# Kernel optimization log

Measured on AMD Instinct MI355X. Metric: run time of the kernel, lower is better.

Reference implementation:

```python
import jax, jax.numpy as jnp
import numpy as np

L, B, C = 512, 64, 512  # seq_len, batch, tags_size


def setup_inputs() -> dict:
    key = jax.random.key(0)
    k1, k2, k3, k4, k5, k6 = jax.random.split(key, 6)
    std = (1.0 / C) ** 0.5
    emit = jax.random.normal(k1, (L, B, C), dtype=jnp.float32)
    trans = jax.random.normal(k2, (C, C), dtype=jnp.float32) * std
    trans_from_start = jax.random.normal(k3, (C,), dtype=jnp.float32) * std
    trans_to_end = jax.random.normal(k4, (C,), dtype=jnp.float32) * std
    target = jax.random.randint(k5, (L, B), 0, C)
    # left-aligned length mask so mask.sum(0)-1 indexes the last valid step
    lens = jax.random.randint(k6, (B,), L // 2, L + 1)
    mask = jnp.arange(L)[:, None] < lens[None, :]
    return {"emit": emit, "target": target, "mask": mask, "trans": trans,
            "trans_from_start": trans_from_start, "trans_to_end": trans_to_end}


def _log_z(emit, mask, trans, trans_from_start, trans_to_end):
    log_alpha0 = emit[0] + trans_from_start  # (B, C)

    def step(log_alpha, xs):
        e_i, m_i = xs  # (B, C), (B,)
        # scores[b, j] = logsumexp_i( log_alpha[b, i] + trans[i, j] + e_i[b, j] )
        s = jax.nn.logsumexp(log_alpha[:, :, None] + trans[None, :, :] + e_i[:, None, :], axis=1)
        log_alpha = jnp.where(m_i[:, None], s, log_alpha)
        return log_alpha, None

    log_alpha, _ = jax.lax.scan(step, log_alpha0, (emit[1:], mask[1:]))
    return jax.nn.logsumexp(log_alpha + trans_to_end, axis=1).sum()


def _score(emit, target, mask, trans, trans_from_start, trans_to_end):
    l, b, c = emit.shape
    tr = trans[target[:-1], target[1:]]  # (L-1, B)
    scores = jnp.concatenate([jnp.zeros((1, b), emit.dtype), tr], axis=0)
    scores = scores + jnp.take_along_axis(emit, target[:, :, None], axis=2)[..., 0]
    score = jnp.where(mask, scores, jnp.zeros((), emit.dtype)).sum()
    ends = mask.sum(axis=0) - 1  # (B,) index of last valid step
    last_tags = target[ends, jnp.arange(b)]
    score = score + trans_from_start[target[0]].sum() + trans_to_end[last_tags].sum()
    return score


def reference(emit, target, mask, trans, trans_from_start, trans_to_end):
    b = emit.shape[1]
    log_z = _log_z(emit, mask, trans, trans_from_start, trans_to_end)
    score = _score(emit, target, mask, trans, trans_from_start, trans_to_end)
    return (log_z - score) / b
```

## Files before the change

### kernel.cpp

```cpp
#include <hip/hip_runtime.h>
#include <hip/hip_bf16.h>
#include <stdint.h>

#define LL 512
#define BB 64
#define CC 512
#define TM 255

typedef float float4v __attribute__((ext_vector_type(4)));
typedef int   int4v   __attribute__((ext_vector_type(4)));
typedef unsigned int uint4v __attribute__((ext_vector_type(4)));
typedef int   int8v  __attribute__((ext_vector_type(8)));

#define WS_ET     262144
#define WS_SCORE  524288
#define WS_SVA    524292
#define WS_SVB    524548
#define WS_CTR    524804
#define WS_ALPHA  528384
#define WS_BETA   659456


__device__ __forceinline__ bool mask_at(const void* maskp, bool is_byte, int t, int b) {
    if (is_byte) return ((const unsigned char*)maskp)[t * BB + b] != 0;
    return ((const int*)maskp)[t * BB + b] != 0;
}

__device__ __forceinline__ float rowmax16_dpp(float x) {
    int t;
    t = __builtin_amdgcn_update_dpp(0, __float_as_int(x), 0x128, 0xF, 0xF, true);
    x = fmaxf(x, __int_as_float(t));
    t = __builtin_amdgcn_update_dpp(0, __float_as_int(x), 0x124, 0xF, 0xF, true);
    x = fmaxf(x, __int_as_float(t));
    t = __builtin_amdgcn_update_dpp(0, __float_as_int(x), 0x122, 0xF, 0xF, true);
    x = fmaxf(x, __int_as_float(t));
    t = __builtin_amdgcn_update_dpp(0, __float_as_int(x), 0x121, 0xF, 0xF, true);
    x = fmaxf(x, __int_as_float(t));
    return x;
}

__device__ __forceinline__ void step_barrier() {
    asm volatile("s_waitcnt lgkmcnt(0)" ::: "memory");
    __builtin_amdgcn_sched_barrier(0);
    __builtin_amdgcn_s_barrier();
    asm volatile("" ::: "memory");
}

__global__ void prep_kernel(const float* __restrict__ trans, unsigned char* __restrict__ ws) {
    int g = blockIdx.x * blockDim.x + threadIdx.x;
    if (g == 0) { *(float*)(ws + WS_SCORE) = 0.0f; *(int*)(ws + WS_CTR) = 0; }
    if (g >= 512 * 128) return;
    int n  = g & 511;
    int pd = g >> 9;
    int wv = pd >> 4, rw = pd & 15;
    float f[4], ft[4];
#pragma unroll
    for (int nt = 0; nt < 4; ++nt) {
        int k = 64 * wv + 16 * nt + rw;
        f[nt]  = __expf(trans[(size_t)k * CC + n]);
        ft[nt] = __expf(trans[(size_t)n * CC + k]);
    }
    int r = 0;
    r = __builtin_amdgcn_cvt_pk_fp8_f32(f[0], f[1], r, false);
    r = __builtin_amdgcn_cvt_pk_fp8_f32(f[2], f[3], r, true);
    ((int*)ws)[n * 128 + pd] = r;
    int r2 = 0;
    r2 = __builtin_amdgcn_cvt_pk_fp8_f32(ft[0], ft[1], r2, false);
    r2 = __builtin_amdgcn_cvt_pk_fp8_f32(ft[2], ft[3], r2, true);
    ((int*)(ws + WS_ET))[n * 128 + pd] = r2;
}

__launch_bounds__(512, 2)
__global__ void crf_scan_kernel(const float* __restrict__ emit,
                                const int* __restrict__ target,
                                const void* __restrict__ maskp,
                                const float* __restrict__ trans,
                                const float* __restrict__ tfs,
                                const float* __restrict__ t2e,
                                unsigned char* __restrict__ ws,
                                float* __restrict__ out) {
    const int tid = threadIdx.x;
    const bool is_byte = ((const unsigned char*)maskp)[1] != 0;

    if (blockIdx.x >= 8) {
        __shared__ float acc8[8];
        int sb = blockIdx.x - 8;
        float val = 0.0f;
        for (int e = sb * 512 + tid; e < LL * BB; e += 32 * 512) {
            int t = e >> 6, b = e & 63;
            if (mask_at(maskp, is_byte, t, b)) {
                int tg  = target[t * BB + b];
                float v = emit[(size_t)(t * BB + b) * CC + tg];
                if (t > 0) v += trans[(size_t)target[(t - 1) * BB + b] * CC + tg];
                val += v;
            }
        }
        if (sb == 0 && tid < BB) {
            int b = tid;
            val += tfs[target[b]];
            int lo = 0, hi = LL;
            while (lo < hi) {
                int mid = (lo + hi) >> 1;
                if (mask_at(maskp, is_byte, mid, b)) lo = mid + 1; else hi = mid;
            }
            val += t2e[target[(lo - 1) * BB + b]];
        }
        for (int off = 32; off > 0; off >>= 1) val += __shfl_down(val, off);
        if ((tid & 63) == 0) atomicAdd((float*)(ws + WS_SCORE), val);
        __syncthreads();
        if (tid == 0) { __threadfence(); atomicAdd((int*)(ws + WS_CTR), 1); }

        if (blockIdx.x == 39) {
            if (tid == 0) {
                while (atomicAdd((int*)(ws + WS_CTR), 0) < 40) __builtin_amdgcn_s_sleep(2);
                __threadfence();
            }
            __syncthreads();
            const int c  = tid >> 3;
            const int s8 = tid & 7;
            const float* A = (const float*)(ws + WS_ALPHA) + (size_t)c * CC;
            const float* B = (const float*)(ws + WS_BETA)  + (size_t)c * CC;
            float d = 0.0f;
            for (int i = s8; i < CC; i += 8) d += A[i] * B[i];
            d += __shfl_xor(d, 1);
            d += __shfl_xor(d, 2);
            d += __shfl_xor(d, 4);
            float v = 0.0f;
            if (s8 == 0)
                v = ((const float*)(ws + WS_SVA))[c] + ((const float*)(ws + WS_SVB))[c] + __logf(d);
            for (int off = 32; off > 0; off >>= 1) v += __shfl_down(v, off);
            if ((tid & 63) == 0) acc8[tid >> 6] = v;
            __syncthreads();
            if (tid == 0) {
                float s = 0.0f;
                for (int i = 0; i < 8; ++i) s += acc8[i];
                out[0] = (s - *(const float*)(ws + WS_SCORE)) * (1.0f / 64.0f);
            }
        }
        return;
    }

    const bool is_fwd = blockIdx.x < 4;
    const int B0 = (is_fwd ? blockIdx.x : blockIdx.x - 4) * 16;

    __shared__ __align__(16) unsigned char p8[2][16 * 528];
    __shared__ __align__(16) float mslotW[2][8][16];
    __shared__ float m0S[16];
    __shared__ float red[16][32];
    __shared__ int   lenS[16];
    __shared__ float mInitS;

    const int wv   = tid >> 6;
    const int lane = tid & 63;
    const int q    = lane >> 4;
    const int r15  = lane & 15;

    const unsigned char* ews = ws + (is_fwd ? 0 : WS_ET);
    int8v ef[4][4];
#pragma unroll
    for (int nt = 0; nt < 4; ++nt) {
        int n = (wv * 4 + nt) * 16 + r15;
#pragma unroll
        for (int kk4 = 0; kk4 < 4; ++kk4) {
            const unsigned char* src = ews + n * 512 + kk4 * 128 + q * 32;
            int4v lo = *(const int4v*)(src);
            int4v hi = *(const int4v*)(src + 16);
            ef[nt][kk4] = __builtin_shufflevector(lo, hi, 0, 1, 2, 3, 4, 5, 6, 7);
        }
    }

    const int c5 = tid >> 5;
    const int s5 = tid & 31;

    if (is_fwd) {
        {
            float lmax = -3.0e38f;
#pragma unroll
            for (int i = 0; i < 4; ++i) {
                int j4 = s5 + 32 * i;
                float4v em = *(const float4v*)(emit + (size_t)(B0 + c5) * CC + 4 * j4);
                float4v tf = *(const float4v*)(tfs + 4 * j4);
                float4v a = em + tf;
                lmax = fmaxf(lmax, fmaxf(fmaxf(a.x, a.y), fmaxf(a.z, a.w)));
            }
            red[c5][s5] = lmax;
        }
        __syncthreads();
        if (tid < 16) {
            float m0 = red[tid][0];
            for (int s = 1; s < 32; ++s) m0 = fmaxf(m0, red[tid][s]);
            m0S[tid] = m0;
        }
        if (tid < 128) ((float*)&mslotW[0][0][0])[tid] = 1.0f;
        __syncthreads();
        {
            float m0 = m0S[c5];
#pragma unroll
            for (int i = 0; i < 4; ++i) {
                int pd = s5 + 32 * i;
                int wvv = pd >> 4, rw = pd & 15;
                float f[4];
#pragma unroll
                for (int nt = 0; nt < 4; ++nt) {
                    int k = 64 * wvv + 16 * nt + rw;
                    f[nt] = __expf(emit[(size_t)(B0 + c5) * CC + k] + tfs[k] - m0);
                }
                int r = 0;
                r = __builtin_amdgcn_cvt_pk_fp8_f32(f[0], f[1], r, false);
                r = __builtin_amdgcn_cvt_pk_fp8_f32(f[2], f[3], r, true);
                *(int*)(&p8[0][0] + c5 * 528 + pd * 4) = r;
            }
        }
        __syncthreads();
    } else {
        {
            float m = t2e[tid];
            for (int off = 32; off > 0; off >>= 1) m = fmaxf(m, __shfl_xor(m, off));
            if (lane == 0) ((float*)red)[wv] = m;
        }
        __syncthreads();
        if (tid == 0) {
            float m = ((float*)red)[0];
            for (int i = 1; i < 8; ++i) m = fmaxf(m, ((float*)red)[i]);
            mInitS = __expf(m);
        }
        __syncthreads();
        {
#pragma unroll
            for (int i = 0; i < 4; ++i) {
                int pd = s5 + 32 * i;
                int wvv = pd >> 4, rw = pd & 15;
                float f[4];
#pragma unroll
                for (int nt = 0; nt < 4; ++nt)
                    f[nt] = __expf(t2e[64 * wvv + 16 * nt + rw]);
                int r = 0;
                r = __builtin_amdgcn_cvt_pk_fp8_f32(f[0], f[1], r, false);
                r = __builtin_amdgcn_cvt_pk_fp8_f32(f[2], f[3], r, true);
                *(int*)(&p8[0][0] + c5 * 528 + pd * 4) = r;
                *(int*)(&p8[1][0] + c5 * 528 + pd * 4) = r;
            }
            int part = 0;
            for (int k = 0; k < 16; ++k)
                part += mask_at(maskp, is_byte, s5 * 16 + k, B0 + c5) ? 1 : 0;
            red[c5][s5] = (float)part;
        }
        __syncthreads();
        if (tid < 16) {
            int s = 0;
            for (int i = 0; i < 32; ++i) s += (int)red[tid][i];
            lenS[tid] = s;
        }
        __syncthreads();
    }

    int4v gsum = {0, 0, 0, 0};
    const float4v z4 = {0.f, 0.f, 0.f, 0.f};

    if (is_fwd) {
        const float* eb0 = emit + (size_t)(BB + B0 + q * 4) * CC + (wv * 64 + r15);
        const float* eb1 = eb0 + 2 * CC;
        float4v ex4[4];
#pragma unroll
        for (int nt = 0; nt < 4; ++nt) {
            ex4[nt][0] = __expf(eb0[0 * CC + nt * 16]);
            ex4[nt][1] = __expf(eb0[1 * CC + nt * 16]);
            ex4[nt][2] = __expf(eb1[0 * CC + nt * 16]);
            ex4[nt][3] = __expf(eb1[1 * CC + nt * 16]);
        }

#pragma unroll 2
        for (int t = 1; t <= TM; ++t) {
            const int wp = t & 1;
            const int rp = wp ^ 1;
            eb0 += BB * CC;
            eb1 += BB * CC;

            const unsigned char* pr = &p8[rp][0] + r15 * 528 + q * 32;
            int8v af[4];
#pragma unroll
            for (int kk4 = 0; kk4 < 4; ++kk4) {
                int4v lo = *(const int4v*)(pr + kk4 * 128);
                int4v hi = *(const int4v*)(pr + kk4 * 128 + 16);
                af[kk4] = __builtin_shufflevector(lo, hi, 0, 1, 2, 3, 4, 5, 6, 7);
            }
            const char* mb = (const char*)&mslotW[(t - 1) & 1][0][q * 4];
            uint4v mm = *(const uint4v*)(mb);
#pragma unroll
            for (int i = 1; i < 8; ++i)
                mm = __builtin_elementwise_max(mm, *(const uint4v*)(mb + i * 64));

            float4v emn4[4];
#pragma unroll
            for (int nt = 0; nt < 4; ++nt) {
                emn4[nt][0] = eb0[0 * CC + nt * 16];
                emn4[nt][1] = eb0[1 * CC + nt * 16];
                emn4[nt][2] = eb1[0 * CC + nt * 16];
                emn4[nt][3] = eb1[1 * CC + nt * 16];
            }

            float4v acc0 = z4, acc1 = z4, acc2 = z4, acc3 = z4;
#pragma unroll
            for (int kk4 = 0; kk4 < 4; ++kk4) {
                acc0 = __builtin_amdgcn_mfma_scale_f32_16x16x128_f8f6f4(
                    af[kk4], ef[0][kk4], acc0, 0, 0, 0, 0x7F7F7F7F, 0, 0x7F7F7F7F);
                acc1 = __builtin_amdgcn_mfma_scale_f32_16x16x128_f8f6f4(
                    af[kk4], ef[1][kk4], acc1, 0, 0, 0, 0x7F7F7F7F, 0, 0x7F7F7F7F);
            }

            int4v e4 = {(int)(mm[0] >> 23), (int)(mm[1] >> 23), (int)(mm[2] >> 23), (int)(mm[3] >> 23)};
            int4v s2b = (248 - e4) << 23;
            float4v s24;
            s24[0] = __int_as_float(s2b[0]); s24[1] = __int_as_float(s2b[1]);
            s24[2] = __int_as_float(s2b[2]); s24[3] = __int_as_float(s2b[3]);

            float4v p0 = acc0 * (ex4[0] * s24);
            float4v p1 = acc1 * (ex4[1] * s24);
            float4v rmA = __builtin_elementwise_max(p0, p1);
            {
                unsigned char* wrow = &p8[wp][0] + (wv * 16 + r15) * 4;
#pragma unroll
                for (int rr = 0; rr < 4; ++rr) {
                    int r = __builtin_amdgcn_cvt_pk_fp8_f32(
                        fminf(p0[rr], 448.0f), fminf(p1[rr], 448.0f), 0, false);
                    *(short*)(wrow + (q * 4 + rr) * 528) = (short)r;
                }
            }
            ex4[0][0] = __expf(emn4[0][0]); ex4[0][1] = __expf(emn4[0][1]);
            ex4[0][2] = __expf(emn4[0][2]); ex4[0][3] = __expf(emn4[0][3]);
            ex4[1][0] = __expf(emn4[1][0]); ex4[1][1] = __expf(emn4[1][1]);
            ex4[1][2] = __expf(emn4[1][2]); ex4[1][3] = __expf(emn4[1][3]);

#pragma unroll
            for (int kk4 = 0; kk4 < 4; ++kk4) {
                acc2 = __builtin_amdgcn_mfma_scale_f32_16x16x128_f8f6f4(
                    af[kk4], ef[2][kk4], acc2, 0, 0, 0, 0x7F7F7F7F, 0, 0x7F7F7F7F);
                acc3 = __builtin_amdgcn_mfma_scale_f32_16x16x128_f8f6f4(
                    af[kk4], ef[3][kk4], acc3, 0, 0, 0, 0x7F7F7F7F, 0, 0x7F7F7F7F);
            }

            float4v p2 = acc2 * (ex4[2] * s24);
            float4v p3 = acc3 * (ex4[3] * s24);
            float4v rmB = __builtin_elementwise_max(p2, p3);
            {
                unsigned char* wrow = &p8[wp][0] + (wv * 16 + r15) * 4;
#pragma unroll
                for (int rr = 0; rr < 4; ++rr) {
                    int r = __builtin_amdgcn_cvt_pk_fp8_f32(
                        fminf(p2[rr], 448.0f), fminf(p3[rr], 448.0f), 0, false);
                    *(short*)(wrow + (q * 4 + rr) * 528 + 2) = (short)r;
                }
            }
            ex4[2][0] = __expf(emn4[2][0]); ex4[2][1] = __expf(emn4[2][1]);
            ex4[2][2] = __expf(emn4[2][2]); ex4[2][3] = __expf(emn4[2][3]);
            ex4[3][0] = __expf(emn4[3][0]); ex4[3][1] = __expf(emn4[3][1]);
            ex4[3][2] = __expf(emn4[3][2]); ex4[3][3] = __expf(emn4[3][3]);

            {
                float4v rm4 = __builtin_elementwise_max(rmA, rmB);
                float4v rw;
#pragma unroll
                for (int rr = 0; rr < 4; ++rr) rw[rr] = rowmax16_dpp(rm4[rr]);
                if (r15 == 0)
                    *(float4v*)&mslotW[t & 1][wv][q * 4] = rw;
            }

            gsum += (e4 - 121);

            if (t == TM) {
                float* wA = (float*)(ws + WS_ALPHA) + (size_t)(B0 + q * 4) * CC + (wv * 64 + r15);
#pragma unroll
                for (int rr = 0; rr < 4; ++rr) {
                    wA[(size_t)rr * CC +  0] = p0[rr];
                    wA[(size_t)rr * CC + 16] = p1[rr];
                    wA[(size_t)rr * CC + 32] = p2[rr];
                    wA[(size_t)rr * CC + 48] = p3[rr];
                }
            }
            step_barrier();
        }
        if (wv == 0 && r15 == 0) {
#pragma unroll
            for (int rr = 0; rr < 4; ++rr)
                ((float*)(ws + WS_SVA))[B0 + q * 4 + rr] =
                    m0S[q * 4 + rr] + 0.6931471805599453f * (float)gsum[rr];
        }
    } else {
        int lenR[4];
#pragma unroll
        for (int rr = 0; rr < 4; ++rr) lenR[rr] = lenS[q * 4 + rr];
        const int eInit = __float_as_int(mInitS) >> 23;

        int rInit = 0;
        rInit = __builtin_amdgcn_cvt_pk_fp8_f32(__expf(t2e[64 * wv + r15]),
                                                __expf(t2e[64 * wv + 16 + r15]), rInit, false);
        rInit = __builtin_amdgcn_cvt_pk_fp8_f32(__expf(t2e[64 * wv + 32 + r15]),
                                                __expf(t2e[64 * wv + 48 + r15]), rInit, true);
        const short rInitLo = (short)(rInit & 0xffff);
        const short rInitHi = (short)(((unsigned)rInit) >> 16);

        const float* eb0 = emit + ((size_t)(LL - 1) * BB + B0 + q * 4) * CC + (wv * 64 + r15);
        const float* eb1 = eb0 + 2 * CC;
        float4v ex4[4];
#pragma unroll
        for (int nt = 0; nt < 4; ++nt) {
            ex4[nt][0] = __expf(eb0[0 * CC + nt * 16]);
            ex4[nt][1] = __expf(eb0[1 * CC + nt * 16]);
            ex4[nt][2] = __expf(eb1[0 * CC + nt * 16]);
            ex4[nt][3] = __expf(eb1[1 * CC + nt * 16]);
        }

#pragma unroll 2
        for (int it = 0; it < 256; ++it) {
            const int t  = 510 - it;
            const int wp = it & 1;
            const int rp = wp ^ 1;
            eb0 -= BB * CC;
            eb1 -= BB * CC;

            const unsigned char* pr = &p8[rp][0] + r15 * 528 + q * 32;
            int8v af[4];
#pragma unroll
            for (int kk4 = 0; kk4 < 4; ++kk4) {
                int4v lo = *(const int4v*)(pr + kk4 * 128);
                int4v hi = *(const int4v*)(pr + kk4 * 128 + 16);
                af[kk4] = __builtin_shufflevector(lo, hi, 0, 1, 2, 3, 4, 5, 6, 7);
            }
            const char* mb = (const char*)&mslotW[(it - 1) & 1][0][q * 4];
            uint4v mm = *(const uint4v*)(mb);
#pragma unroll
            for (int i = 1; i < 8; ++i)
                mm = __builtin_elementwise_max(mm, *(const uint4v*)(mb + i * 64));

            float4v emn4[4];
#pragma unroll
            for (int nt = 0; nt < 4; ++nt) {
                emn4[nt][0] = eb0[0 * CC + nt * 16];
                emn4[nt][1] = eb0[1 * CC + nt * 16];
                emn4[nt][2] = eb1[0 * CC + nt * 16];
                emn4[nt][3] = eb1[1 * CC + nt * 16];
            }

            float4v acc0 = z4, acc1 = z4, acc2 = z4, acc3 = z4;
#pragma unroll
            for (int kk4 = 0; kk4 < 4; ++kk4) {
                acc0 = __builtin_amdgcn_mfma_scale_f32_16x16x128_f8f6f4(
                    af[kk4], ef[0][kk4], acc0, 0, 0, 0, 0x7F7F7F7F, 0, 0x7F7F7F7F);
                acc1 = __builtin_amdgcn_mfma_scale_f32_16x16x128_f8f6f4(
                    af[kk4], ef[1][kk4], acc1, 0, 0, 0, 0x7F7F7F7F, 0, 0x7F7F7F7F);
            }

            int4v e4 = {(int)(mm[0] >> 23), (int)(mm[1] >> 23), (int)(mm[2] >> 23), (int)(mm[3] >> 23)};
            int4v eU;
            float4v s2U;
            bool lv[4];
#pragma unroll
            for (int rr = 0; rr < 4; ++rr) {
                bool ui = (t >= lenR[rr] - 2);
                lv[rr] = (t <= lenR[rr] - 2);
                int e = ui ? eInit : e4[rr];
                eU[rr] = e;
                s2U[rr] = __int_as_float((248 - e) << 23);
            }

            float4v p0 = acc0 * (ex4[0] * s2U);
            float4v p1 = acc1 * (ex4[1] * s2U);
            float4v rmA = __builtin_elementwise_max(p0, p1);
            {
                unsigned char* wrow = &p8[wp][0] + (wv * 16 + r15) * 4;
#pragma unroll
                for (int rr = 0; rr < 4; ++rr) {
                    int r = __builtin_amdgcn_cvt_pk_fp8_f32(
                        fminf(p0[rr], 448.0f), fminf(p1[rr], 448.0f), 0, false);
                    *(short*)(wrow + (q * 4 + rr) * 528) = lv[rr] ? (short)r : rInitLo;
                }
            }
            ex4[0][0] = __expf(emn4[0][0]); ex4[0][1] = __expf(emn4[0][1]);
            ex4[0][2] = __expf(emn4[0][2]); ex4[0][3] = __expf(emn4[0][3]);
            ex4[1][0] = __expf(emn4[1][0]); ex4[1][1] = __expf(emn4[1][1]);
            ex4[1][2] = __expf(emn4[1][2]); ex4[1][3] = __expf(emn4[1][3]);

#pragma unroll
            for (int kk4 = 0; kk4 < 4; ++kk4) {
                acc2 = __builtin_amdgcn_mfma_scale_f32_16x16x128_f8f6f4(
                    af[kk4], ef[2][kk4], acc2, 0, 0, 0, 0x7F7F7F7F, 0, 0x7F7F7F7F);
                acc3 = __builtin_amdgcn_mfma_scale_f32_16x16x128_f8f6f4(
                    af[kk4], ef[3][kk4], acc3, 0, 0, 0, 0x7F7F7F7F, 0, 0x7F7F7F7F);
            }

            float4v p2 = acc2 * (ex4[2] * s2U);
            float4v p3 = acc3 * (ex4[3] * s2U);
            float4v rmB = __builtin_elementwise_max(p2, p3);
            {
                unsigned char* wrow = &p8[wp][0] + (wv * 16 + r15) * 4;
#pragma unroll
                for (int rr = 0; rr < 4; ++rr) {
                    int r = __builtin_amdgcn_cvt_pk_fp8_f32(
                        fminf(p2[rr], 448.0f), fminf(p3[rr], 448.0f), 0, false);
                    *(short*)(wrow + (q * 4 + rr) * 528 + 2) = lv[rr] ? (short)r : rInitHi;
                }
            }
            ex4[2][0] = __expf(emn4[2][0]); ex4[2][1] = __expf(emn4[2][1]);
            ex4[2][2] = __expf(emn4[2][2]); ex4[2][3] = __expf(emn4[2][3]);
            ex4[3][0] = __expf(emn4[3][0]); ex4[3][1] = __expf(emn4[3][1]);
            ex4[3][2] = __expf(emn4[3][2]); ex4[3][3] = __expf(emn4[3][3]);

            {
                float4v rm4 = __builtin_elementwise_max(rmA, rmB);
                float4v rw;
#pragma unroll
                for (int rr = 0; rr < 4; ++rr) rw[rr] = rowmax16_dpp(rm4[rr]);
                if (r15 == 0)
                    *(float4v*)&mslotW[it & 1][wv][q * 4] = rw;
            }

#pragma unroll
            for (int rr = 0; rr < 4; ++rr)
                gsum[rr] += lv[rr] ? (eU[rr] - 121) : 0;

            if (t == TM) {
                float* wB = (float*)(ws + WS_BETA) + (size_t)(B0 + q * 4) * CC + (wv * 64 + r15);
#pragma unroll
                for (int nt = 0; nt < 4; ++nt) {
                    float e2 = __expf(t2e[wv * 64 + nt * 16 + r15]);
                    const float4v& psel = (nt == 0) ? p0 : (nt == 1) ? p1 : (nt == 2) ? p2 : p3;
#pragma unroll
                    for (int rr = 0; rr < 4; ++rr)
                        wB[(size_t)rr * CC + nt * 16] = lv[rr] ? psel[rr] : e2;
                }
            }
            step_barrier();
        }
        if (wv == 0 && r15 == 0) {
#pragma unroll
            for (int rr = 0; rr < 4; ++rr)
                ((float*)(ws + WS_SVB))[B0 + q * 4 + rr] =
                    0.6931471805599453f * (float)gsum[rr];
        }
    }

    __syncthreads();
    if (tid == 0) { __threadfence(); atomicAdd((int*)(ws + WS_CTR), 1); }
}

extern "C" void kernel_launch(void* const* d_in, const int* in_sizes, int n_in,
                              void* d_out, int out_size, void* d_ws, size_t ws_size,
                              hipStream_t stream) {
    const float* emit   = (const float*)d_in[0];
    const int*   target = (const int*)d_in[1];
    const void*  maskp  = d_in[2];
    const float* trans  = (const float*)d_in[3];
    const float* tfs    = (const float*)d_in[4];
    const float* t2e    = (const float*)d_in[5];
    unsigned char* ws   = (unsigned char*)d_ws;
    float* out          = (float*)d_out;

    prep_kernel<<<256, 256, 0, stream>>>(trans, ws);
    crf_scan_kernel<<<40, 512, 0, stream>>>(emit, target, maskp, trans, tfs, t2e, ws, out);
}
```

Before: 567.3 us.

## Double scan block width to 16 waves, stream trans fragments from memory, split combine kernel

The forward/backward scan blocks go from 8 to 16 waves, so each wave handles 32 output tags (two MFMA tiles) instead of 64 per step. Transition fragments are no longer held in registers; they are reloaded each step from the workspace with software-prefetched double buffering. The final combine moves from a spin-waiting block into a separate small kernel, which removes the atomic counter. This aims to shorten the per-step critical path of the serial scan through more parallelism, at the cost of more global/L2 traffic per step and a wider cross-wave max reduction across 16 slots.

Result: slower. 2.062 ms (+263.4%).

```diff
diff --git a/kernel.cpp b/kernel.cpp
--- a/kernel.cpp
+++ b/kernel.cpp
@@ -14,9 +14,8 @@
 
 #define WS_ET     262144
 #define WS_SCORE  524288
-#define WS_SVA    524292
-#define WS_SVB    524548
-#define WS_CTR    524804
+#define WS_SVA    524352
+#define WS_SVB    524608
 #define WS_ALPHA  528384
 #define WS_BETA   659456
 
@@ -48,7 +47,7 @@
 
 __global__ void prep_kernel(const float* __restrict__ trans, unsigned char* __restrict__ ws) {
     int g = blockIdx.x * blockDim.x + threadIdx.x;
-    if (g == 0) { *(float*)(ws + WS_SCORE) = 0.0f; *(int*)(ws + WS_CTR) = 0; }
+    if (g == 0) *(float*)(ws + WS_SCORE) = 0.0f;
     if (g >= 512 * 128) return;
     int n  = g & 511;
     int pd = g >> 9;
@@ -70,23 +69,21 @@
     ((int*)(ws + WS_ET))[n * 128 + pd] = r2;
 }
 
-__launch_bounds__(512, 2)
+__launch_bounds__(1024, 4)
 __global__ void crf_scan_kernel(const float* __restrict__ emit,
                                 const int* __restrict__ target,
                                 const void* __restrict__ maskp,
                                 const float* __restrict__ trans,
                                 const float* __restrict__ tfs,
                                 const float* __restrict__ t2e,
-                                unsigned char* __restrict__ ws,
-                                float* __restrict__ out) {
+                                unsigned char* __restrict__ ws) {
     const int tid = threadIdx.x;
     const bool is_byte = ((const unsigned char*)maskp)[1] != 0;
 
     if (blockIdx.x >= 8) {
-        __shared__ float acc8[8];
         int sb = blockIdx.x - 8;
         float val = 0.0f;
-        for (int e = sb * 512 + tid; e < LL * BB; e += 32 * 512) {
+        for (int e = sb * 1024 + tid; e < LL * BB; e += 32 * 1024) {
             int t = e >> 6, b = e & 63;
             if (mask_at(maskp, is_byte, t, b)) {
                 int tg  = target[t * BB + b];
@@ -107,36 +104,6 @@
         }
         for (int off = 32; off > 0; off >>= 1) val += __shfl_down(val, off);
         if ((tid & 63) == 0) atomicAdd((float*)(ws + WS_SCORE), val);
-        __syncthreads();
-        if (tid == 0) { __threadfence(); atomicAdd((int*)(ws + WS_CTR), 1); }
-
-        if (blockIdx.x == 39) {
-            if (tid == 0) {
-                while (atomicAdd((int*)(ws + WS_CTR), 0) < 40) __builtin_amdgcn_s_sleep(2);
-                __threadfence();
-            }
-            __syncthreads();
-            const int c  = tid >> 3;
-            const int s8 = tid & 7;
-            const float* A = (const float*)(ws + WS_ALPHA) + (size_t)c * CC;
-            const float* B = (const float*)(ws + WS_BETA)  + (size_t)c * CC;
-            float d = 0.0f;
-            for (int i = s8; i < CC; i += 8) d += A[i] * B[i];
-            d += __shfl_xor(d, 1);
-            d += __shfl_xor(d, 2);
-            d += __shfl_xor(d, 4);
-            float v = 0.0f;
-            if (s8 == 0)
-                v = ((const float*)(ws + WS_SVA))[c] + ((const float*)(ws + WS_SVB))[c] + __logf(d);
-            for (int off = 32; off > 0; off >>= 1) v += __shfl_down(v, off);
-            if ((tid & 63) == 0) acc8[tid >> 6] = v;
-            __syncthreads();
-            if (tid == 0) {
-                float s = 0.0f;
-                for (int i = 0; i < 8; ++i) s += acc8[i];
-                out[0] = (s - *(const float*)(ws + WS_SCORE)) * (1.0f / 64.0f);
-            }
-        }
         return;
     }
 
@@ -144,7 +111,7 @@
     const int B0 = (is_fwd ? blockIdx.x : blockIdx.x - 4) * 16;
 
     __shared__ __align__(16) unsigned char p8[2][16 * 528];
-    __shared__ __align__(16) float mslotW[2][8][16];
+    __shared__ __align__(16) float mslotW[2][16][16];
     __shared__ float m0S[16];
     __shared__ float red[16][32];
     __shared__ int   lenS[16];
@@ -154,26 +121,11 @@
     const int lane = tid & 63;
     const int q    = lane >> 4;
     const int r15  = lane & 15;
-
-    const unsigned char* ews = ws + (is_fwd ? 0 : WS_ET);
-    int8v ef[4][4];
-#pragma unroll
-    for (int nt = 0; nt < 4; ++nt) {
-        int n = (wv * 4 + nt) * 16 + r15;
-#pragma unroll
-        for (int kk4 = 0; kk4 < 4; ++kk4) {
-            const unsigned char* src = ews + n * 512 + kk4 * 128 + q * 32;
-            int4v lo = *(const int4v*)(src);
-            int4v hi = *(const int4v*)(src + 16);
-            ef[nt][kk4] = __builtin_shufflevector(lo, hi, 0, 1, 2, 3, 4, 5, 6, 7);
-        }
-    }
-
-    const int c5 = tid >> 5;
-    const int s5 = tid & 31;
+    const int c5   = tid >> 5;
+    const int s5   = tid & 31;
 
     if (is_fwd) {
-        {
+        if (tid < 512) {
             float lmax = -3.0e38f;
 #pragma unroll
             for (int i = 0; i < 4; ++i) {
@@ -191,9 +143,9 @@
             for (int s = 1; s < 32; ++s) m0 = fmaxf(m0, red[tid][s]);
             m0S[tid] = m0;
         }
-        if (tid < 128) ((float*)&mslotW[0][0][0])[tid] = 1.0f;
-        __syncthreads();
-        {
+        if (tid < 256) ((float*)&mslotW[0][0][0])[tid] = 1.0f;
+        __syncthreads();
+        if (tid < 512) {
             float m0 = m0S[c5];
 #pragma unroll
             for (int i = 0; i < 4; ++i) {
@@ -213,7 +165,7 @@
         }
         __syncthreads();
     } else {
-        {
+        if (tid < 512) {
             float m = t2e[tid];
             for (int off = 32; off > 0; off >>= 1) m = fmaxf(m, __shfl_xor(m, off));
             if (lane == 0) ((float*)red)[wv] = m;
@@ -225,7 +177,7 @@
             mInitS = __expf(m);
         }
         __syncthreads();
-        {
+        if (tid < 512) {
 #pragma unroll
             for (int i = 0; i < 4; ++i) {
                 int pd = s5 + 32 * i;
@@ -254,59 +206,42 @@
         __syncthreads();
     }
 
+    const unsigned char* ews = ws + (is_fwd ? 0 : WS_ET);
+    const unsigned char* pA = ews + (size_t)(wv * 32 + r15) * 512 + q * 32;
+    const unsigned char* pB = pA + 16 * 512;
+    const int wcol = (wv >> 1) * 64 + r15 * 4 + (wv & 1) * 2;
+
     int4v gsum = {0, 0, 0, 0};
     const float4v z4 = {0.f, 0.f, 0.f, 0.f};
 
     if (is_fwd) {
-        const float* eb0 = emit + (size_t)(BB + B0 + q * 4) * CC + (wv * 64 + r15);
+        const float* eb0 = emit + (size_t)(BB + B0 + q * 4) * CC + (wv * 32 + r15);
         const float* eb1 = eb0 + 2 * CC;
-        float4v ex4[4];
-#pragma unroll
-        for (int nt = 0; nt < 4; ++nt) {
-            ex4[nt][0] = __expf(eb0[0 * CC + nt * 16]);
-            ex4[nt][1] = __expf(eb0[1 * CC + nt * 16]);
-            ex4[nt][2] = __expf(eb1[0 * CC + nt * 16]);
-            ex4[nt][3] = __expf(eb1[1 * CC + nt * 16]);
-        }
-
-#pragma unroll 2
+        float exv[8];
+        exv[0] = __expf(eb0[0]);  exv[1] = __expf(eb0[CC]);
+        exv[2] = __expf(eb1[0]);  exv[3] = __expf(eb1[CC]);
+        exv[4] = __expf(eb0[16]); exv[5] = __expf(eb0[CC + 16]);
+        exv[6] = __expf(eb1[16]); exv[7] = __expf(eb1[CC + 16]);
+
+#pragma unroll 1
         for (int t = 1; t <= TM; ++t) {
-            const int wp = t & 1;
-            const int rp = wp ^ 1;
+            const int wp = t & 1, rp = wp ^ 1;
             eb0 += BB * CC;
             eb1 += BB * CC;
 
             const unsigned char* pr = &p8[rp][0] + r15 * 528 + q * 32;
-            int8v af[4];
-#pragma unroll
-            for (int kk4 = 0; kk4 < 4; ++kk4) {
-                int4v lo = *(const int4v*)(pr + kk4 * 128);
-                int4v hi = *(const int4v*)(pr + kk4 * 128 + 16);
-                af[kk4] = __builtin_shufflevector(lo, hi, 0, 1, 2, 3, 4, 5, 6, 7);
-            }
+
             const char* mb = (const char*)&mslotW[(t - 1) & 1][0][q * 4];
             uint4v mm = *(const uint4v*)(mb);
 #pragma unroll
-            for (int i = 1; i < 8; ++i)
+            for (int i = 1; i < 16; ++i)
                 mm = __builtin_elementwise_max(mm, *(const uint4v*)(mb + i * 64));
 
-            float4v emn4[4];
-#pragma unroll
-            for (int nt = 0; nt < 4; ++nt) {
-                emn4[nt][0] = eb0[0 * CC + nt * 16];
-                emn4[nt][1] = eb0[1 * CC + nt * 16];
-                emn4[nt][2] = eb1[0 * CC + nt * 16];
-                emn4[nt][3] = eb1[1 * CC + nt * 16];
-            }
-
-            float4v acc0 = z4, acc1 = z4, acc2 = z4, acc3 = z4;
-#pragma unroll
-            for (int kk4 = 0; kk4 < 4; ++kk4) {
-                acc0 = __builtin_amdgcn_mfma_scale_f32_16x16x128_f8f6f4(
-                    af[kk4], ef[0][kk4], acc0, 0, 0, 0, 0x7F7F7F7F, 0, 0x7F7F7F7F);
-                acc1 = __builtin_amdgcn_mfma_scale_f32_16x16x128_f8f6f4(
-                    af[kk4], ef[1][kk4], acc1, 0, 0, 0, 0x7F7F7F7F, 0, 0x7F7F7F7F);
-            }
+            float emn[8];
+            emn[0] = eb0[0];  emn[1] = eb0[CC];
+            emn[2] = eb1[0];  emn[3] = eb1[CC];
+            emn[4] = eb0[16]; emn[5] = eb0[CC + 16];
+            emn[6] = eb1[16]; emn[7] = eb1[CC + 16];
 
             int4v e4 = {(int)(mm[0] >> 23), (int)(mm[1] >> 23), (int)(mm[2] >> 23), (int)(mm[3] >> 23)};
             int4v s2b = (248 - e4) << 23;
@@ -314,11 +249,58 @@
             s24[0] = __int_as_float(s2b[0]); s24[1] = __int_as_float(s2b[1]);
             s24[2] = __int_as_float(s2b[2]); s24[3] = __int_as_float(s2b[3]);
 
-            float4v p0 = acc0 * (ex4[0] * s24);
-            float4v p1 = acc1 * (ex4[1] * s24);
-            float4v rmA = __builtin_elementwise_max(p0, p1);
+            float4v acc0 = z4, acc1 = z4;
+            int4v afl[2], afh[2], eal[2], eah[2], ebl[2], ebh[2];
+            afl[0] = *(const int4v*)(pr);       afh[0] = *(const int4v*)(pr + 16);
+            eal[0] = *(const int4v*)(pA);       eah[0] = *(const int4v*)(pA + 16);
+            ebl[0] = *(const int4v*)(pB);       ebh[0] = *(const int4v*)(pB + 16);
+#pragma unroll
+            for (int k = 0; k < 4; ++k) {
+                const int cur = k & 1, nxt = cur ^ 1;
+                if (k < 3) {
+                    afl[nxt] = *(const int4v*)(pr + (k + 1) * 128);
+                    afh[nxt] = *(const int4v*)(pr + (k + 1) * 128 + 16);
+                    eal[nxt] = *(const int4v*)(pA + (k + 1) * 128);
+                    eah[nxt] = *(const int4v*)(pA + (k + 1) * 128 + 16);
+                    ebl[nxt] = *(const int4v*)(pB + (k + 1) * 128);
+                    ebh[nxt] = *(const int4v*)(pB + (k + 1) * 128 + 16);
+                }
+                int8v af = __builtin_shufflevector(afl[cur], afh[cur], 0, 1, 2, 3, 4, 5, 6, 7);
+                int8v eA = __builtin_shufflevector(eal[cur], eah[cur], 0, 1, 2, 3, 4, 5, 6, 7);
+                int8v eB = __builtin_shufflevector(ebl[cur], ebh[cur], 0, 1, 2, 3, 4, 5, 6, 7);
+                acc0 = __builtin_amdgcn_mfma_scale_f32_16x16x128_f8f6f4(
+                    af, eA, acc0, 0, 0, 0, 0x7F7F7F7F, 0, 0x7F7F7F7F);
+                acc1 = __builtin_amdgcn_mfma_scale_f32_16x16x128_f8f6f4(
+                    af, eB, acc1, 0, 0, 0, 0x7F7F7F7F, 0, 0x7F7F7F7F);
+            }
+
+            float4v p0, p1;
+#pragma unroll
+            for (int rr = 0; rr < 4; ++rr) {
+                p0[rr] = acc0[rr] * (exv[rr] * s24[rr]);
+                p1[rr] = acc1[rr] * (exv[4 + rr] * s24[rr]);
+            }
+
+            if (t == TM) {
+                float* wA = (float*)(ws + WS_ALPHA) + (size_t)(B0 + q * 4) * CC + (wv * 32 + r15);
+#pragma unroll
+                for (int rr = 0; rr < 4; ++rr) {
+                    wA[(size_t)rr * CC + 0]  = p0[rr];
+                    wA[(size_t)rr * CC + 16] = p1[rr];
+                }
+            }
+
             {
-                unsigned char* wrow = &p8[wp][0] + (wv * 16 + r15) * 4;
+                float4v rm4 = __builtin_elementwise_max(p0, p1);
+                float4v rw;
+#pragma unroll
+                for (int rr = 0; rr < 4; ++rr) rw[rr] = rowmax16_dpp(rm4[rr]);
+                if (r15 == 0)
+                    *(float4v*)&mslotW[t & 1][wv][q * 4] = rw;
+            }
+
+            {
+                unsigned char* wrow = &p8[wp][0] + wcol;
 #pragma unroll
                 for (int rr = 0; rr < 4; ++rr) {
                     int r = __builtin_amdgcn_cvt_pk_fp8_f32(
@@ -326,57 +308,11 @@
                     *(short*)(wrow + (q * 4 + rr) * 528) = (short)r;
                 }
             }
-            ex4[0][0] = __expf(emn4[0][0]); ex4[0][1] = __expf(emn4[0][1]);
-            ex4[0][2] = __expf(emn4[0][2]); ex4[0][3] = __expf(emn4[0][3]);
-            ex4[1][0] = __expf(emn4[1][0]); ex4[1][1] = __expf(emn4[1][1]);
-            ex4[1][2] = __expf(emn4[1][2]); ex4[1][3] = __expf(emn4[1][3]);
-
-#pragma unroll
-            for (int kk4 = 0; kk4 < 4; ++kk4) {
-                acc2 = __builtin_amdgcn_mfma_scale_f32_16x16x128_f8f6f4(
-                    af[kk4], ef[2][kk4], acc2, 0, 0, 0, 0x7F7F7F7F, 0, 0x7F7F7F7F);
-                acc3 = __builtin_amdgcn_mfma_scale_f32_16x16x128_f8f6f4(
-                    af[kk4], ef[3][kk4], acc3, 0, 0, 0, 0x7F7F7F7F, 0, 0x7F7F7F7F);
-            }
-
-            float4v p2 = acc2 * (ex4[2] * s24);
-            float4v p3 = acc3 * (ex4[3] * s24);
-            float4v rmB = __builtin_elementwise_max(p2, p3);
-            {
-                unsigned char* wrow = &p8[wp][0] + (wv * 16 + r15) * 4;
-#pragma unroll
-                for (int rr = 0; rr < 4; ++rr) {
-                    int r = __builtin_amdgcn_cvt_pk_fp8_f32(
-                        fminf(p2[rr], 448.0f), fminf(p3[rr], 448.0f), 0, false);
-                    *(short*)(wrow + (q * 4 + rr) * 528 + 2) = (short)r;
-                }
-            }
-            ex4[2][0] = __expf(emn4[2][0]); ex4[2][1] = __expf(emn4[2][1]);
-            ex4[2][2] = __expf(emn4[2][2]); ex4[2][3] = __expf(emn4[2][3]);
-            ex4[3][0] = __expf(emn4[3][0]); ex4[3][1] = __expf(emn4[3][1]);
-            ex4[3][2] = __expf(emn4[3][2]); ex4[3][3] = __expf(emn4[3][3]);
-
-            {
-                float4v rm4 = __builtin_elementwise_max(rmA, rmB);
-                float4v rw;
-#pragma unroll
-                for (int rr = 0; rr < 4; ++rr) rw[rr] = rowmax16_dpp(rm4[rr]);
-                if (r15 == 0)
-                    *(float4v*)&mslotW[t & 1][wv][q * 4] = rw;
-            }
 
             gsum += (e4 - 121);
 
-            if (t == TM) {
-                float* wA = (float*)(ws + WS_ALPHA) + (size_t)(B0 + q * 4) * CC + (wv * 64 + r15);
-#pragma unroll
-                for (int rr = 0; rr < 4; ++rr) {
-                    wA[(size_t)rr * CC +  0] = p0[rr];
-                    wA[(size_t)rr * CC + 16] = p1[rr];
-                    wA[(size_t)rr * CC + 32] = p2[rr];
-                    wA[(size_t)rr * CC + 48] = p3[rr];
-                }
-            }
+#pragma unroll
+            for (int i = 0; i < 8; ++i) exv[i] = __expf(emn[i]);
             step_barrier();
         }
         if (wv == 0 && r15 == 0) {
@@ -390,65 +326,37 @@
 #pragma unroll
         for (int rr = 0; rr < 4; ++rr) lenR[rr] = lenS[q * 4 + rr];
         const int eInit = __float_as_int(mInitS) >> 23;
-
-        int rInit = 0;
-        rInit = __builtin_amdgcn_cvt_pk_fp8_f32(__expf(t2e[64 * wv + r15]),
-                                                __expf(t2e[64 * wv + 16 + r15]), rInit, false);
-        rInit = __builtin_amdgcn_cvt_pk_fp8_f32(__expf(t2e[64 * wv + 32 + r15]),
-                                                __expf(t2e[64 * wv + 48 + r15]), rInit, true);
-        const short rInitLo = (short)(rInit & 0xffff);
-        const short rInitHi = (short)(((unsigned)rInit) >> 16);
-
-        const float* eb0 = emit + ((size_t)(LL - 1) * BB + B0 + q * 4) * CC + (wv * 64 + r15);
+        const float e2a = __expf(t2e[wv * 32 + r15]);
+        const float e2b = __expf(t2e[wv * 32 + 16 + r15]);
+
+        const float* eb0 = emit + ((size_t)(LL - 1) * BB + B0 + q * 4) * CC + (wv * 32 + r15);
         const float* eb1 = eb0 + 2 * CC;
-        float4v ex4[4];
-#pragma unroll
-        for (int nt = 0; nt < 4; ++nt) {
-            ex4[nt][0] = __expf(eb0[0 * CC + nt * 16]);
-            ex4[nt][1] = __expf(eb0[1 * CC + nt * 16]);
-            ex4[nt][2] = __expf(eb1[0 * CC + nt * 16]);
-            ex4[nt][3] = __expf(eb1[1 * CC + nt * 16]);
-        }
-
-#pragma unroll 2
+        float exv[8];
+        exv[0] = __expf(eb0[0]);  exv[1] = __expf(eb0[CC]);
+        exv[2] = __expf(eb1[0]);  exv[3] = __expf(eb1[CC]);
+        exv[4] = __expf(eb0[16]); exv[5] = __expf(eb0[CC + 16]);
+        exv[6] = __expf(eb1[16]); exv[7] = __expf(eb1[CC + 16]);
+
+#pragma unroll 1
         for (int it = 0; it < 256; ++it) {
             const int t  = 510 - it;
-            const int wp = it & 1;
-            const int rp = wp ^ 1;
+            const int wp = it & 1, rp = wp ^ 1;
             eb0 -= BB * CC;
             eb1 -= BB * CC;
 
             const unsigned char* pr = &p8[rp][0] + r15 * 528 + q * 32;
-            int8v af[4];
-#pragma unroll
-            for (int kk4 = 0; kk4 < 4; ++kk4) {
-                int4v lo = *(const int4v*)(pr + kk4 * 128);
-                int4v hi = *(const int4v*)(pr + kk4 * 128 + 16);
-                af[kk4] = __builtin_shufflevector(lo, hi, 0, 1, 2, 3, 4, 5, 6, 7);
-            }
+
             const char* mb = (const char*)&mslotW[(it - 1) & 1][0][q * 4];
             uint4v mm = *(const uint4v*)(mb);
 #pragma unroll
-            for (int i = 1; i < 8; ++i)
+            for (int i = 1; i < 16; ++i)
                 mm = __builtin_elementwise_max(mm, *(const uint4v*)(mb + i * 64));
 
-            float4v emn4[4];
-#pragma unroll
-            for (int nt = 0; nt < 4; ++nt) {
-                emn4[nt][0] = eb0[0 * CC + nt * 16];
-                emn4[nt][1] = eb0[1 * CC + nt * 16];
-                emn4[nt][2] = eb1[0 * CC + nt * 16];
-                emn4[nt][3] = eb1[1 * CC + nt * 16];
-            }
-
-            float4v acc0 = z4, acc1 = z4, acc2 = z4, acc3 = z4;
-#pragma unroll
-            for (int kk4 = 0; kk4 < 4; ++kk4) {
-                acc0 = __builtin_amdgcn_mfma_scale_f32_16x16x128_f8f6f4(
-                    af[kk4], ef[0][kk4], acc0, 0, 0, 0, 0x7F7F7F7F, 0, 0x7F7F7F7F);
-                acc1 = __builtin_amdgcn_mfma_scale_f32_16x16x128_f8f6f4(
-                    af[kk4], ef[1][kk4], acc1, 0, 0, 0, 0x7F7F7F7F, 0, 0x7F7F7F7F);
-            }
+            float emn[8];
+            emn[0] = eb0[0];  emn[1] = eb0[CC];
+            emn[2] = eb1[0];  emn[3] = eb1[CC];
+            emn[4] = eb0[16]; emn[5] = eb0[CC + 16];
+            emn[6] = eb1[16]; emn[7] = eb1[CC + 16];
 
             int4v e4 = {(int)(mm[0] >> 23), (int)(mm[1] >> 23), (int)(mm[2] >> 23), (int)(mm[3] >> 23)};
             int4v eU;
@@ -463,72 +371,73 @@
                 s2U[rr] = __int_as_float((248 - e) << 23);
             }
 
-            float4v p0 = acc0 * (ex4[0] * s2U);
-            float4v p1 = acc1 * (ex4[1] * s2U);
-            float4v rmA = __builtin_elementwise_max(p0, p1);
+            float4v acc0 = z4, acc1 = z4;
+            int4v afl[2], afh[2], eal[2], eah[2], ebl[2], ebh[2];
+            afl[0] = *(const int4v*)(pr);       afh[0] = *(const int4v*)(pr + 16);
+            eal[0] = *(const int4v*)(pA);       eah[0] = *(const int4v*)(pA + 16);
+            ebl[0] = *(const int4v*)(pB);       ebh[0] = *(const int4v*)(pB + 16);
+#pragma unroll
+            for (int k = 0; k < 4; ++k) {
+                const int cur = k & 1, nxt = cur ^ 1;
+                if (k < 3) {
+                    afl[nxt] = *(const int4v*)(pr + (k + 1) * 128);
+                    afh[nxt] = *(const int4v*)(pr + (k + 1) * 128 + 16);
+                    eal[nxt] = *(const int4v*)(pA + (k + 1) * 128);
+                    eah[nxt] = *(const int4v*)(pA + (k + 1) * 128 + 16);
+                    ebl[nxt] = *(const int4v*)(pB + (k + 1) * 128);
+                    ebh[nxt] = *(const int4v*)(pB + (k + 1) * 128 + 16);
+                }
+                int8v af = __builtin_shufflevector(afl[cur], afh[cur], 0, 1, 2, 3, 4, 5, 6, 7);
+                int8v eA = __builtin_shufflevector(eal[cur], eah[cur], 0, 1, 2, 3, 4, 5, 6, 7);
+                int8v eB = __builtin_shufflevector(ebl[cur], ebh[cur], 0, 1, 2, 3, 4, 5, 6, 7);
+                acc0 = __builtin_amdgcn_mfma_scale_f32_16x16x128_f8f6f4(
+                    af, eA, acc0, 0, 0, 0, 0x7F7F7F7F, 0, 0x7F7F7F7F);
+                acc1 = __builtin_amdgcn_mfma_scale_f32_16x16x128_f8f6f4(
+                    af, eB, acc1, 0, 0, 0, 0x7F7F7F7F, 0, 0x7F7F7F7F);
+            }
+
+            float4v p0, p1;
+#pragma unroll
+            for (int rr = 0; rr < 4; ++rr) {
+                p0[rr] = acc0[rr] * (exv[rr] * s2U[rr]);
+                p1[rr] = acc1[rr] * (exv[4 + rr] * s2U[rr]);
+            }
+
+            if (t == TM) {
+                float* wB = (float*)(ws + WS_BETA) + (size_t)(B0 + q * 4) * CC + (wv * 32 + r15);
+#pragma unroll
+                for (int rr = 0; rr < 4; ++rr) {
+                    wB[(size_t)rr * CC + 0]  = lv[rr] ? p0[rr] : e2a;
+                    wB[(size_t)rr * CC + 16] = lv[rr] ? p1[rr] : e2b;
+                }
+            }
+
             {
-                unsigned char* wrow = &p8[wp][0] + (wv * 16 + r15) * 4;
+                float4v rm4 = __builtin_elementwise_max(p0, p1);
+                float4v rw;
+#pragma unroll
+                for (int rr = 0; rr < 4; ++rr) rw[rr] = rowmax16_dpp(rm4[rr]);
+                if (r15 == 0)
+                    *(float4v*)&mslotW[it & 1][wv][q * 4] = rw;
+            }
+
+            {
+                unsigned char* wrow = &p8[wp][0] + wcol;
 #pragma unroll
                 for (int rr = 0; rr < 4; ++rr) {
                     int r = __builtin_amdgcn_cvt_pk_fp8_f32(
                         fminf(p0[rr], 448.0f), fminf(p1[rr], 448.0f), 0, false);
-                    *(short*)(wrow + (q * 4 + rr) * 528) = lv[rr] ? (short)r : rInitLo;
-                }
-            }
-            ex4[0][0] = __expf(emn4[0][0]); ex4[0][1] = __expf(emn4[0][1]);
-            ex4[0][2] = __expf(emn4[0][2]); ex4[0][3] = __expf(emn4[0][3]);
-            ex4[1][0] = __expf(emn4[1][0]); ex4[1][1] = __expf(emn4[1][1]);
-            ex4[1][2] = __expf(emn4[1][2]); ex4[1][3] = __expf(emn4[1][3]);
-
-#pragma unroll
-            for (int kk4 = 0; kk4 < 4; ++kk4) {
-                acc2 = __builtin_amdgcn_mfma_scale_f32_16x16x128_f8f6f4(
-                    af[kk4], ef[2][kk4], acc2, 0, 0, 0, 0x7F7F7F7F, 0, 0x7F7F7F7F);
-                acc3 = __builtin_amdgcn_mfma_scale_f32_16x16x128_f8f6f4(
-                    af[kk4], ef[3][kk4], acc3, 0, 0, 0, 0x7F7F7F7F, 0, 0x7F7F7F7F);
-            }
-
-            float4v p2 = acc2 * (ex4[2] * s2U);
-            float4v p3 = acc3 * (ex4[3] * s2U);
-            float4v rmB = __builtin_elementwise_max(p2, p3);
-            {
-                unsigned char* wrow = &p8[wp][0] + (wv * 16 + r15) * 4;
-#pragma unroll
-                for (int rr = 0; rr < 4; ++rr) {
-                    int r = __builtin_amdgcn_cvt_pk_fp8_f32(
-                        fminf(p2[rr], 448.0f), fminf(p3[rr], 448.0f), 0, false);
-                    *(short*)(wrow + (q * 4 + rr) * 528 + 2) = lv[rr] ? (short)r : rInitHi;
-                }
-            }
-            ex4[2][0] = __expf(emn4[2][0]); ex4[2][1] = __expf(emn4[2][1]);
-            ex4[2][2] = __expf(emn4[2][2]); ex4[2][3] = __expf(emn4[2][3]);
-            ex4[3][0] = __expf(emn4[3][0]); ex4[3][1] = __expf(emn4[3][1]);
-            ex4[3][2] = __expf(emn4[3][2]); ex4[3][3] = __expf(emn4[3][3]);
-
-            {
-                float4v rm4 = __builtin_elementwise_max(rmA, rmB);
-                float4v rw;
-#pragma unroll
-                for (int rr = 0; rr < 4; ++rr) rw[rr] = rowmax16_dpp(rm4[rr]);
-                if (r15 == 0)
-                    *(float4v*)&mslotW[it & 1][wv][q * 4] = rw;
+                    if (lv[rr])
+                        *(short*)(wrow + (q * 4 + rr) * 528) = (short)r;
+                }
             }
 
 #pragma unroll
             for (int rr = 0; rr < 4; ++rr)
                 gsum[rr] += lv[rr] ? (eU[rr] - 121) : 0;
 
-            if (t == TM) {
-                float* wB = (float*)(ws + WS_BETA) + (size_t)(B0 + q * 4) * CC + (wv * 64 + r15);
-#pragma unroll
-                for (int nt = 0; nt < 4; ++nt) {
-                    float e2 = __expf(t2e[wv * 64 + nt * 16 + r15]);
-                    const float4v& psel = (nt == 0) ? p0 : (nt == 1) ? p1 : (nt == 2) ? p2 : p3;
-#pragma unroll
-                    for (int rr = 0; rr < 4; ++rr)
-                        wB[(size_t)rr * CC + nt * 16] = lv[rr] ? psel[rr] : e2;
-                }
-            }
+#pragma unroll
+            for (int i = 0; i < 8; ++i) exv[i] = __expf(emn[i]);
             step_barrier();
         }
         if (wv == 0 && r15 == 0) {
@@ -538,9 +447,31 @@
                     0.6931471805599453f * (float)gsum[rr];
         }
     }
-
+}
+
+__global__ void combine_kernel(const unsigned char* __restrict__ ws, float* __restrict__ out) {
+    __shared__ float acc8[8];
+    const int tid = threadIdx.x;
+    const int c  = tid >> 3;
+    const int s8 = tid & 7;
+    const float* A = (const float*)(ws + WS_ALPHA) + (size_t)c * CC;
+    const float* B = (const float*)(ws + WS_BETA)  + (size_t)c * CC;
+    float d = 0.0f;
+    for (int i = s8; i < CC; i += 8) d += A[i] * B[i];
+    d += __shfl_xor(d, 1);
+    d += __shfl_xor(d, 2);
+    d += __shfl_xor(d, 4);
+    float v = 0.0f;
+    if (s8 == 0)
+        v = ((const float*)(ws + WS_SVA))[c] + ((const float*)(ws + WS_SVB))[c] + __logf(d);
+    for (int off = 32; off > 0; off >>= 1) v += __shfl_down(v, off);
+    if ((tid & 63) == 0) acc8[tid >> 6] = v;
     __syncthreads();
-    if (tid == 0) { __threadfence(); atomicAdd((int*)(ws + WS_CTR), 1); }
+    if (tid == 0) {
+        float s = 0.0f;
+        for (int i = 0; i < 8; ++i) s += acc8[i];
+        out[0] = (s - *(const float*)(ws + WS_SCORE)) * (1.0f / 64.0f);
+    }
 }
 
 extern "C" void kernel_launch(void* const* d_in, const int* in_sizes, int n_in,
@@ -556,5 +487,6 @@
     float* out          = (float*)d_out;
 
     prep_kernel<<<256, 256, 0, stream>>>(trans, ws);
-    crf_scan_kernel<<<40, 512, 0, stream>>>(emit, target, maskp, trans, tfs, t2e, ws, out);
-}
+    crf_scan_kernel<<<40, 1024, 0, stream>>>(emit, target, maskp, trans, tfs, t2e, ws);
+    combine_kernel<<<1, 512, 0, stream>>>(ws, out);
+}
```
